# Performance work log

Hardware: AMD Instinct MI355X
Metric: run time of the kernel (lower is better)

Reference implementation:

```python
import jax, jax.numpy as jnp
import numpy as np

N_STEPS = 6
LN_EPS = 1e-5

def _lin(x, w, b):
    # torch Linear: y = x @ W^T + b, w: [out, in]
    return jnp.matmul(x, w.T) + b

def _gelu(x):
    return jax.nn.gelu(x, approximate=False)

def setup_inputs() -> dict:
    key = jax.random.key(0)
    B, T, D, C, V, MS = 8, 1024, 512, 512, 32000, 1024
    ks = jax.random.split(key, 16)
    w = lambda k, shape: (jax.random.normal(k, shape, jnp.float32) * 0.02)
    return {
        "tokens": jax.random.randint(ks[0], (B, T), 0, V),
        "c_states": jax.random.normal(ks[1], (4, C), jnp.float32),
        "embed_w": w(ks[2], (V, D)),
        "pos_w": w(ks[3], (MS, D)),
        "cn_w1": w(ks[4], (2 * D, 4 * D)), "cn_b1": jnp.zeros((2 * D,), jnp.float32),
        "cn_w2": w(ks[5], (D, 2 * D)), "cn_b2": jnp.zeros((D,), jnp.float32),
        "ent_w1": w(ks[6], (64, D)), "ent_b1": jnp.zeros((64,), jnp.float32),
        "ent_w2": w(ks[7], (1, 64)), "ent_b2": jnp.zeros((1,), jnp.float32),
        "ctc_w1": w(ks[8], (2 * D, C)), "ctc_b1": jnp.zeros((2 * D,), jnp.float32),
        "ctc_w2": w(ks[9], (D, 2 * D)), "ctc_b2": jnp.zeros((D,), jnp.float32),
        "base_temp": jnp.asarray(2.0, jnp.float32),
        "ln_g": jnp.ones((D,), jnp.float32), "ln_b": jnp.zeros((D,), jnp.float32),
        "head_w": w(ks[10], (V, D)),
    }

def reference(tokens, c_states, embed_w, pos_w, cn_w1, cn_b1, cn_w2, cn_b2,
              ent_w1, ent_b1, ent_w2, ent_b2, ctc_w1, ctc_b1, ctc_w2, ctc_b2,
              base_temp, ln_g, ln_b, head_w):
    B, T = tokens.shape
    x = embed_w[tokens] + pos_w[:T][None, :, :]          # [B,T,D]
    c_pooled = c_states.mean(axis=0)                      # [C]
    c_constraint = _lin(_gelu(_lin(c_pooled, ctc_w1, ctc_b1)), ctc_w2, ctc_b2)  # [D]
    c_exp = jnp.broadcast_to(c_constraint, (B, T, c_constraint.shape[0]))
    sp_temp = jax.nn.softplus(base_temp)
    for step in range(N_STEPS):
        temp = sp_temp * (1.0 - step / N_STEPS * 0.8)
        left = jnp.roll(x, 1, axis=1)
        right = jnp.roll(x, -1, axis=1)
        ci = jnp.concatenate([x, left, right, c_exp], axis=-1)  # [B,T,4D]
        constraint = _lin(_gelu(_lin(ci, cn_w1, cn_b1)), cn_w2, cn_b2)  # [B,T,D]
        entropy = _lin(_gelu(_lin(x, ent_w1, ent_b1)), ent_w2, ent_b2)[..., 0]  # [B,T]
        cw = jax.nn.softmax(-entropy / temp, axis=-1)            # softmax over T
        x = x + constraint * cw[..., None] * 0.3
    mu = x.mean(axis=-1, keepdims=True)
    var = ((x - mu) ** 2).mean(axis=-1, keepdims=True)
    xn = (x - mu) * jax.lax.rsqrt(var + LN_EPS) * ln_g + ln_b
    return jnp.matmul(xn, head_w.T)                        # [B,T,V]
```

## Files before the change

### kernel.cpp

```cpp
#include <hip/hip_runtime.h>
#include <hip/hip_bf16.h>

typedef __hip_bfloat16 bf16_t;
typedef __bf16 bf16x8_t __attribute__((ext_vector_type(8)));
typedef float f32x4_t __attribute__((ext_vector_type(4)));

#define OFF_X     ((size_t)0)
#define OFF_XB    ((size_t)16777216)
#define OFF_H1    ((size_t)25165824)
#define OFF_XN    ((size_t)41943040)
#define OFF_HEADB ((size_t)50331648)
#define OFF_W1B   ((size_t)83099648)
#define OFF_W2B   ((size_t)86245376)
#define OFF_EW1   ((size_t)87293952)
#define OFF_ENT   ((size_t)87359488)
#define OFF_CW    ((size_t)87392256)
#define OFF_HC    ((size_t)87425024)
#define OFF_CC    ((size_t)87429120)
#define OFF_B1    ((size_t)87431168)

__device__ __forceinline__ float gelu_f(float v) {
    return 0.5f * v * (1.0f + erff(v * 0.7071067811865475f));
}

__device__ __forceinline__ void load_lds16(const bf16_t* g, bf16_t* l) {
    __builtin_amdgcn_global_load_lds(
        (const __attribute__((address_space(1))) void*)g,
        (__attribute__((address_space(3))) void*)l, 16, 0, 0);
}

#define BAR()    __builtin_amdgcn_s_barrier()
#define SCHED0() __builtin_amdgcn_sched_barrier(0)
#define LGKM0()  asm volatile("s_waitcnt lgkmcnt(0)" ::: "memory")
#define WAITV0() asm volatile("s_waitcnt vmcnt(0)" ::: "memory")
#define WAITV2() asm volatile("s_waitcnt vmcnt(2)" ::: "memory")
#define WAITV4() asm volatile("s_waitcnt vmcnt(4)" ::: "memory")

__global__ void prep1_kernel(const float* __restrict__ cs, const float* __restrict__ w1,
                             const float* __restrict__ b1, float* __restrict__ hc) {
    int o = blockIdx.x * 256 + threadIdx.x;
    const float* wr = w1 + (size_t)o * 512;
    float acc = 0.f;
    for (int k = 0; k < 512; k += 4) {
        float4 w4 = *(const float4*)(wr + k);
        float4 a = *(const float4*)(cs + k);
        float4 b = *(const float4*)(cs + 512 + k);
        float4 c = *(const float4*)(cs + 1024 + k);
        float4 d = *(const float4*)(cs + 1536 + k);
        acc += w4.x * (a.x + b.x + c.x + d.x) * 0.25f;
        acc += w4.y * (a.y + b.y + c.y + d.y) * 0.25f;
        acc += w4.z * (a.z + b.z + c.z + d.z) * 0.25f;
        acc += w4.w * (a.w + b.w + c.w + d.w) * 0.25f;
    }
    hc[o] = gelu_f(acc + b1[o]);
}

__global__ void prep2_kernel(const float* __restrict__ hc, const float* __restrict__ w2,
                             const float* __restrict__ b2, float* __restrict__ cc) {
    int o = blockIdx.x * 256 + threadIdx.x;
    const float* wr = w2 + (size_t)o * 1024;
    float acc = 0.f;
    for (int k = 0; k < 1024; ++k) acc += wr[k] * hc[k];
    cc[o] = acc + b2[o];
}

__global__ void prep3_kernel(const float* __restrict__ cc, const float* __restrict__ cn_w1,
                             const float* __restrict__ cn_b1, float* __restrict__ bias1) {
    int o = blockIdx.x * 256 + threadIdx.x;
    const float* wr = cn_w1 + (size_t)o * 2048 + 1536;
    float acc = 0.f;
    for (int k = 0; k < 512; ++k) acc += wr[k] * cc[k];
    bias1[o] = acc + cn_b1[o];
}

__global__ void embed_kernel(const int* __restrict__ tokens, const float* __restrict__ ew,
                             const float* __restrict__ pw, float* __restrict__ x,
                             bf16_t* __restrict__ xb) {
    int idx = blockIdx.x * 256 + threadIdx.x;
    int d4 = idx & 127;
    int bt = idx >> 7;
    int t = bt & 1023;
    int tok = tokens[bt];
    float4 e = ((const float4*)(ew + (size_t)tok * 512))[d4];
    float4 p = ((const float4*)(pw + (size_t)t * 512))[d4];
    float4 o = make_float4(e.x + p.x, e.y + p.y, e.z + p.z, e.w + p.w);
    ((float4*)x)[idx] = o;
    __hip_bfloat162 p0, p1;
    p0.x = __float2bfloat16(o.x); p0.y = __float2bfloat16(o.y);
    p1.x = __float2bfloat16(o.z); p1.y = __float2bfloat16(o.w);
    ((__hip_bfloat162*)xb)[idx * 2]     = p0;
    ((__hip_bfloat162*)xb)[idx * 2 + 1] = p1;
}

__global__ void cvt_kernel(const float* __restrict__ src, bf16_t* __restrict__ dst) {
    int idx = blockIdx.x * 256 + threadIdx.x;
    float4 v = ((const float4*)src)[idx];
    __hip_bfloat162 p0, p1;
    p0.x = __float2bfloat16(v.x); p0.y = __float2bfloat16(v.y);
    p1.x = __float2bfloat16(v.z); p1.y = __float2bfloat16(v.w);
    ((__hip_bfloat162*)dst)[idx * 2]     = p0;
    ((__hip_bfloat162*)dst)[idx * 2 + 1] = p1;
}

__global__ void cvt_w1_kernel(const float* __restrict__ w1, bf16_t* __restrict__ dst) {
    int idx = blockIdx.x * 256 + threadIdx.x;
    int k4 = idx % 384;
    int o = idx / 384;
    float4 v = ((const float4*)(w1 + (size_t)o * 2048))[k4];
    __hip_bfloat162 p0, p1;
    p0.x = __float2bfloat16(v.x); p0.y = __float2bfloat16(v.y);
    p1.x = __float2bfloat16(v.z); p1.y = __float2bfloat16(v.w);
    ((__hip_bfloat162*)dst)[idx * 2]     = p0;
    ((__hip_bfloat162*)dst)[idx * 2 + 1] = p1;
}

__global__ __launch_bounds__(256) void entropy_mfma(
        const bf16_t* __restrict__ xb, const bf16_t* __restrict__ w1b,
        const float* __restrict__ b1, const float* __restrict__ w2,
        const float* __restrict__ b2, float* __restrict__ ent) {
    int wave = threadIdx.x >> 6, lane = threadIdx.x & 63;
    int lr = lane & 15, kq = lane >> 4;
    int tok0 = (blockIdx.x * 4 + wave) * 16;
    f32x4_t acc[4] = {};
    const bf16_t* xr = xb + (size_t)(tok0 + lr) * 512 + kq * 8;
    const bf16_t* wr = w1b + (size_t)lr * 512 + kq * 8;
    #pragma unroll 4
    for (int k0 = 0; k0 < 512; k0 += 32) {
        bf16x8_t a = *(const bf16x8_t*)(xr + k0);
        #pragma unroll
        for (int j = 0; j < 4; ++j) {
            bf16x8_t bb = *(const bf16x8_t*)(wr + (size_t)j * 16 * 512 + k0);
            acc[j] = __builtin_amdgcn_mfma_f32_16x16x32_bf16(a, bb, acc[j], 0, 0, 0);
        }
    }
    float p[4];
    #pragma unroll
    for (int r = 0; r < 4; ++r) {
        float s = 0.f;
        #pragma unroll
        for (int j = 0; j < 4; ++j) {
            int n = j * 16 + lr;
            s += gelu_f(acc[j][r] + b1[n]) * w2[n];
        }
        #pragma unroll
        for (int o = 1; o < 16; o <<= 1) s += __shfl_xor(s, o);
        p[r] = s;
    }
    if (lr == 0) {
        float bb = b2[0];
        #pragma unroll
        for (int r = 0; r < 4; ++r) ent[tok0 + kq * 4 + r] = p[r] + bb;
    }
}

__global__ void softmax_kernel(const float* __restrict__ ent, const float* __restrict__ btp,
                               float stepf, float* __restrict__ cw) {
    __shared__ float red[16];
    __shared__ float bc[2];
    int b = blockIdx.x, t = threadIdx.x;
    float bt = btp[0];
    float sp = (bt > 20.0f) ? bt : log1pf(expf(bt));
    float inv = -1.0f / (sp * stepf);
    float v = ent[b * 1024 + t] * inv;
    float m = v;
    #pragma unroll
    for (int o = 32; o; o >>= 1) m = fmaxf(m, __shfl_xor(m, o));
    if ((t & 63) == 0) red[t >> 6] = m;
    __syncthreads();
    if (t < 64) {
        float mm = (t < 16) ? red[t] : -3.4e38f;
        #pragma unroll
        for (int o = 32; o; o >>= 1) mm = fmaxf(mm, __shfl_xor(mm, o));
        if (t == 0) bc[0] = mm;
    }
    __syncthreads();
    float e = expf(v - bc[0]);
    float s = e;
    #pragma unroll
    for (int o = 32; o; o >>= 1) s += __shfl_xor(s, o);
    if ((t & 63) == 0) red[t >> 6] = s;
    __syncthreads();
    if (t < 64) {
        float ss = (t < 16) ? red[t] : 0.f;
        #pragma unroll
        for (int o = 32; o; o >>= 1) ss += __shfl_xor(ss, o);
        if (t == 0) bc[1] = ss;
    }
    __syncthreads();
    cw[b * 1024 + t] = e / bc[1];
}

__global__ void ln_kernel(const float* __restrict__ x, const float* __restrict__ g,
                          const float* __restrict__ b, bf16_t* __restrict__ xn) {
    int token = blockIdx.x * 4 + (threadIdx.x >> 6);
    int l = threadIdx.x & 63;
    const float* xr = x + (size_t)token * 512;
    float4 v0 = ((const float4*)xr)[l * 2];
    float4 v1 = ((const float4*)xr)[l * 2 + 1];
    float s = v0.x + v0.y + v0.z + v0.w + v1.x + v1.y + v1.z + v1.w;
    float ss = v0.x * v0.x + v0.y * v0.y + v0.z * v0.z + v0.w * v0.w
             + v1.x * v1.x + v1.y * v1.y + v1.z * v1.z + v1.w * v1.w;
    #pragma unroll
    for (int o = 32; o; o >>= 1) { s += __shfl_xor(s, o); ss += __shfl_xor(ss, o); }
    float mu = s * (1.0f / 512.0f);
    float var = ss * (1.0f / 512.0f) - mu * mu;
    float rs = rsqrtf(var + 1e-5f);
    float4 g0 = ((const float4*)g)[l * 2], g1 = ((const float4*)g)[l * 2 + 1];
    float4 b0 = ((const float4*)b)[l * 2], b1 = ((const float4*)b)[l * 2 + 1];
    bf16_t* op = xn + (size_t)token * 512 + l * 8;
    op[0] = __float2bfloat16((v0.x - mu) * rs * g0.x + b0.x);
    op[1] = __float2bfloat16((v0.y - mu) * rs * g0.y + b0.y);
    op[2] = __float2bfloat16((v0.z - mu) * rs * g0.z + b0.z);
    op[3] = __float2bfloat16((v0.w - mu) * rs * g0.w + b0.w);
    op[4] = __float2bfloat16((v1.x - mu) * rs * g1.x + b1.x);
    op[5] = __float2bfloat16((v1.y - mu) * rs * g1.y + b1.y);
    op[6] = __float2bfloat16((v1.z - mu) * rs * g1.z + b1.z);
    op[7] = __float2bfloat16((v1.w - mu) * rs * g1.w + b1.w);
}

template <int MODE, int ROLL, int BN>
__global__ __launch_bounds__(512, 2) void gemm8p(
    const bf16_t* __restrict__ A, int lda,
    const bf16_t* __restrict__ B, int ldb, int K, int NMT,
    const float* __restrict__ bias,
    bf16_t* __restrict__ out_bf, int ldc,
    const float* __restrict__ cw, float* __restrict__ x,
    float* __restrict__ out_f)
{
    constexpr int JJ = BN / 64;
    __shared__ __align__(16) bf16_t As[2][256 * 64];
    __shared__ __align__(16) bf16_t Bs[2][BN * 64];

    const int NT = K >> 6;
    const int nwg = gridDim.x;
    const int id0 = blockIdx.x;
    const int id = (id0 & 7) * (nwg >> 3) + (id0 >> 3);
    const int m0 = (id % NMT) * 256;
    const int n0 = (id / NMT) * BN;

    const int tid = threadIdx.x;
    const int wave = tid >> 6, lane = tid & 63;
    const int wm = (wave >> 2) * 128;
    const int wn = (wave & 3) * (BN / 4);
    const int lr = lane & 15, kq = lane >> 4;

    const int swz0 = (kq)     ^ (lr & 7);
    const int swz1 = (4 + kq) ^ (lr & 7);
    const int eoff0 = lr * 64 + swz0 * 8;
    const int eoff1 = lr * 64 + swz1 * 8;

    const int u0row = tid >> 3;
    const int u1row = 64 + (tid >> 3);
    const int usl   = tid & 7;
    const int c0 = ((usl ^ (u0row & 7)) * 8);
    const int c1 = ((usl ^ (u1row & 7)) * 8);

    f32x4_t acc[8][JJ] = {};
    bf16x8_t bfr[JJ][2];

    auto stageA = [&](int ktile, int c, int half) {
        const int kbase = ktile << 6;
        const int r0 = m0 + half * 128 + u0row;
        const int r1 = m0 + half * 128 + u1row;
        const bf16_t *g0, *g1;
        if (ROLL) {
            const int seg = kbase >> 9;
            const int kk2 = kbase & 511;
            const int sh = (seg == 0) ? 0 : ((seg == 1) ? 1023 : 1);
            const int s0 = (r0 & ~1023) | (((r0 & 1023) + sh) & 1023);
            const int s1 = (r1 & ~1023) | (((r1 & 1023) + sh) & 1023);
            g0 = A + (size_t)s0 * 512 + kk2 + c0;
            g1 = A + (size_t)s1 * 512 + kk2 + c1;
        } else {
            g0 = A + (size_t)r0 * lda + kbase + c0;
            g1 = A + (size_t)r1 * lda + kbase + c1;
        }
        bf16_t* l = &As[c][half * 128 * 64];
        load_lds16(g0, l + tid * 8);
        load_lds16(g1, l + (tid + 512) * 8);
    };
    auto stageB = [&](int ktile, int c, int half) {
        const int kbase = ktile << 6;
        const int r0 = n0 + half * 128 + u0row;
        const int r1 = n0 + half * 128 + u1row;
        const bf16_t* g0 = B + (size_t)r0 * ldb + kbase + c0;
        const bf16_t* g1 = B + (size_t)r1 * ldb + kbase + c1;
        bf16_t* l = &Bs[c][half * 128 * 64];
        load_lds16(g0, l + tid * 8);
        load_lds16(g1, l + (tid + 512) * 8);
    };

    stageA(0, 0, 0); stageA(0, 0, 1);
    stageB(0, 0, 0); if (BN == 256) stageB(0, 0, 1);
    stageB(1, 1, 0); if (BN == 256) stageB(1, 1, 1);
    if (BN == 256) { WAITV4(); } else { WAITV2(); }
    BAR();

    int cur = 0;
    for (int t = 0; t < NT; ++t) {
        #pragma unroll
        for (int p = 0; p < 4; ++p) {
            bf16x8_t af0k0, af0k1, af1k0, af1k1;
            {
                const int r0 = (wm + 32 * p + lr) * 64;
                const int r1 = (wm + 32 * p + 16 + lr) * 64;
                af0k0 = *(const bf16x8_t*)&As[cur][r0 - lr * 64 + eoff0];
                af0k1 = *(const bf16x8_t*)&As[cur][r0 - lr * 64 + eoff1];
                af1k0 = *(const bf16x8_t*)&As[cur][r1 - lr * 64 + eoff0];
                af1k1 = *(const bf16x8_t*)&As[cur][r1 - lr * 64 + eoff1];
            }
            if (p == 0) {
                #pragma unroll
                for (int j = 0; j < JJ; ++j) {
                    const int rb = (wn + 16 * j) * 64;
                    bfr[j][0] = *(const bf16x8_t*)&Bs[cur][rb + eoff0];
                    bfr[j][1] = *(const bf16x8_t*)&Bs[cur][rb + eoff1];
                }
            }
            if (p == 0 && t + 1 < NT) stageA(t + 1, cur ^ 1, 0);
            if (p == 1 && t + 1 < NT) stageA(t + 1, cur ^ 1, 1);
            if (p == 2 && t + 2 < NT) stageB(t + 2, cur, 0);
            if (p == 3 && BN == 256 && t + 2 < NT) stageB(t + 2, cur, 1);

            BAR();
            LGKM0();
            SCHED0();
            __builtin_amdgcn_s_setprio(1);
            #pragma unroll
            for (int j = 0; j < JJ; ++j) {
                acc[2*p][j]   = __builtin_amdgcn_mfma_f32_16x16x32_bf16(af0k0, bfr[j][0], acc[2*p][j],   0, 0, 0);
                acc[2*p+1][j] = __builtin_amdgcn_mfma_f32_16x16x32_bf16(af1k0, bfr[j][0], acc[2*p+1][j], 0, 0, 0);
            }
            #pragma unroll
            for (int j = 0; j < JJ; ++j) {
                acc[2*p][j]   = __builtin_amdgcn_mfma_f32_16x16x32_bf16(af0k1, bfr[j][1], acc[2*p][j],   0, 0, 0);
                acc[2*p+1][j] = __builtin_amdgcn_mfma_f32_16x16x32_bf16(af1k1, bfr[j][1], acc[2*p+1][j], 0, 0, 0);
            }
            __builtin_amdgcn_s_setprio(0);
            SCHED0();
            if (p == 3) {
                if (t + 2 < NT) { if (BN == 256) { WAITV4(); } else { WAITV2(); } }
                else           { WAITV0(); }
            }
            BAR();
        }
        cur ^= 1;
    }

    #pragma unroll
    for (int i = 0; i < 8; ++i) {
        const int rbase = m0 + wm + i * 16 + kq * 4;
        #pragma unroll
        for (int j = 0; j < JJ; ++j) {
            const int gcol = n0 + wn + j * 16 + lr;
            #pragma unroll
            for (int r = 0; r < 4; ++r) {
                const size_t grow = (size_t)(rbase + r);
                float v = acc[i][j][r];
                if (MODE == 0) {
                    v = gelu_f(v + bias[gcol]);
                    out_bf[grow * ldc + gcol] = __float2bfloat16(v);
                } else if (MODE == 1) {
                    v += bias[gcol];
                    float nv = x[grow * ldc + gcol] + v * cw[grow] * 0.3f;
                    x[grow * ldc + gcol] = nv;
                    out_bf[grow * ldc + gcol] = __float2bfloat16(nv);
                } else {
                    out_f[grow * ldc + gcol] = v;
                }
            }
        }
    }
}

extern "C" void kernel_launch(void* const* d_in, const int* in_sizes, int n_in,
                              void* d_out, int out_size, void* d_ws, size_t ws_size,
                              hipStream_t stream) {
    const int*   tokens   = (const int*)d_in[0];
    const float* c_states = (const float*)d_in[1];
    const float* embed_w  = (const float*)d_in[2];
    const float* pos_w    = (const float*)d_in[3];
    const float* cn_w1    = (const float*)d_in[4];
    const float* cn_b1    = (const float*)d_in[5];
    const float* cn_w2    = (const float*)d_in[6];
    const float* cn_b2    = (const float*)d_in[7];
    const float* ent_w1   = (const float*)d_in[8];
    const float* ent_b1   = (const float*)d_in[9];
    const float* ent_w2   = (const float*)d_in[10];
    const float* ent_b2   = (const float*)d_in[11];
    const float* ctc_w1   = (const float*)d_in[12];
    const float* ctc_b1   = (const float*)d_in[13];
    const float* ctc_w2   = (const float*)d_in[14];
    const float* ctc_b2   = (const float*)d_in[15];
    const float* base_temp= (const float*)d_in[16];
    const float* ln_g     = (const float*)d_in[17];
    const float* ln_b     = (const float*)d_in[18];
    const float* head_w   = (const float*)d_in[19];
    float* out = (float*)d_out;

    char* ws = (char*)d_ws;
    float*  x     = (float*)(ws + OFF_X);
    bf16_t* xb    = (bf16_t*)(ws + OFF_XB);
    bf16_t* h1    = (bf16_t*)(ws + OFF_H1);
    bf16_t* xn    = (bf16_t*)(ws + OFF_XN);
    bf16_t* headb = (bf16_t*)(ws + OFF_HEADB);
    bf16_t* w1b   = (bf16_t*)(ws + OFF_W1B);
    bf16_t* w2b   = (bf16_t*)(ws + OFF_W2B);
    bf16_t* ew1b  = (bf16_t*)(ws + OFF_EW1);
    float*  ent   = (float*)(ws + OFF_ENT);
    float*  cw    = (float*)(ws + OFF_CW);
    float*  hc    = (float*)(ws + OFF_HC);
    float*  cc    = (float*)(ws + OFF_CC);
    float*  bias1 = (float*)(ws + OFF_B1);

    cvt_w1_kernel<<<1536, 256, 0, stream>>>(cn_w1, w1b);
    cvt_kernel<<<512, 256, 0, stream>>>(cn_w2, w2b);
    cvt_kernel<<<32, 256, 0, stream>>>(ent_w1, ew1b);
    prep1_kernel<<<4, 256, 0, stream>>>(c_states, ctc_w1, ctc_b1, hc);
    prep2_kernel<<<2, 256, 0, stream>>>(hc, ctc_w2, ctc_b2, cc);
    prep3_kernel<<<4, 256, 0, stream>>>(cc, cn_w1, cn_b1, bias1);
    embed_kernel<<<4096, 256, 0, stream>>>(tokens, embed_w, pos_w, x, xb);

    for (int step = 0; step < 6; ++step) {
        float stepf = 1.0f - ((float)step / 6.0f) * 0.8f;
        entropy_mfma<<<128, 256, 0, stream>>>(xb, ew1b, ent_b1, ent_w2, ent_b2, ent);
        softmax_kernel<<<8, 1024, 0, stream>>>(ent, base_temp, stepf, cw);
        gemm8p<0, 1, 128><<<256, 512, 0, stream>>>(xb, 512, w1b, 1536, 1536, 32,
                                                   bias1, h1, 1024, nullptr, nullptr, nullptr);
        gemm8p<1, 0, 128><<<128, 512, 0, stream>>>(h1, 1024, w2b, 1024, 1024, 32,
                                                   cn_b2, xb, 512, cw, x, nullptr);
    }

    cvt_kernel<<<16000, 256, 0, stream>>>(head_w, headb);
    ln_kernel<<<2048, 256, 0, stream>>>(x, ln_g, ln_b, xn);
    gemm8p<2, 0, 256><<<4000, 512, 0, stream>>>(xn, 512, headb, 512, 512, 32,
                                                nullptr, nullptr, 32000, nullptr, nullptr, out);
}
```

Baseline: 1.205 ms.

## Fuse entropy into first GEMM, softmax into second, merge prep and convert kernels

The entropy MLP now runs as extra workgroups appended to the first constraint GEMM launch. Each block of the second GEMM recomputes the per-batch softmax over T from the entropy values and keeps its slice of the weights in shared memory. This removes two launches per step and the cw buffer round trip. The three small prep matvecs become one single-block kernel that holds intermediates in LDS, and all weight conversions merge into one launch. The cost is redundant softmax work in every GEMM block, plus a serial single-block prep kernel.

```diff
diff --git a/kernel.cpp b/kernel.cpp
--- a/kernel.cpp
+++ b/kernel.cpp
@@ -14,10 +14,7 @@
 #define OFF_W2B   ((size_t)86245376)
 #define OFF_EW1   ((size_t)87293952)
 #define OFF_ENT   ((size_t)87359488)
-#define OFF_CW    ((size_t)87392256)
-#define OFF_HC    ((size_t)87425024)
-#define OFF_CC    ((size_t)87429120)
-#define OFF_B1    ((size_t)87431168)
+#define OFF_B1    ((size_t)87425024)
 
 __device__ __forceinline__ float gelu_f(float v) {
     return 0.5f * v * (1.0f + erff(v * 0.7071067811865475f));
@@ -36,41 +33,45 @@
 #define WAITV2() asm volatile("s_waitcnt vmcnt(2)" ::: "memory")
 #define WAITV4() asm volatile("s_waitcnt vmcnt(4)" ::: "memory")
 
-__global__ void prep1_kernel(const float* __restrict__ cs, const float* __restrict__ w1,
-                             const float* __restrict__ b1, float* __restrict__ hc) {
-    int o = blockIdx.x * 256 + threadIdx.x;
-    const float* wr = w1 + (size_t)o * 512;
-    float acc = 0.f;
-    for (int k = 0; k < 512; k += 4) {
-        float4 w4 = *(const float4*)(wr + k);
-        float4 a = *(const float4*)(cs + k);
-        float4 b = *(const float4*)(cs + 512 + k);
-        float4 c = *(const float4*)(cs + 1024 + k);
-        float4 d = *(const float4*)(cs + 1536 + k);
-        acc += w4.x * (a.x + b.x + c.x + d.x) * 0.25f;
-        acc += w4.y * (a.y + b.y + c.y + d.y) * 0.25f;
-        acc += w4.z * (a.z + b.z + c.z + d.z) * 0.25f;
-        acc += w4.w * (a.w + b.w + c.w + d.w) * 0.25f;
-    }
-    hc[o] = gelu_f(acc + b1[o]);
-}
-
-__global__ void prep2_kernel(const float* __restrict__ hc, const float* __restrict__ w2,
-                             const float* __restrict__ b2, float* __restrict__ cc) {
-    int o = blockIdx.x * 256 + threadIdx.x;
-    const float* wr = w2 + (size_t)o * 1024;
-    float acc = 0.f;
-    for (int k = 0; k < 1024; ++k) acc += wr[k] * hc[k];
-    cc[o] = acc + b2[o];
-}
-
-__global__ void prep3_kernel(const float* __restrict__ cc, const float* __restrict__ cn_w1,
-                             const float* __restrict__ cn_b1, float* __restrict__ bias1) {
-    int o = blockIdx.x * 256 + threadIdx.x;
-    const float* wr = cn_w1 + (size_t)o * 2048 + 1536;
-    float acc = 0.f;
-    for (int k = 0; k < 512; ++k) acc += wr[k] * cc[k];
-    bias1[o] = acc + cn_b1[o];
+__global__ __launch_bounds__(1024) void prep_all(
+        const float* __restrict__ cs,
+        const float* __restrict__ ctc_w1, const float* __restrict__ ctc_b1,
+        const float* __restrict__ ctc_w2, const float* __restrict__ ctc_b2,
+        const float* __restrict__ cn_w1, const float* __restrict__ cn_b1,
+        float* __restrict__ bias1) {
+    __shared__ float hc_s[1024];
+    __shared__ float cc_s[512];
+    int o = threadIdx.x;
+    {
+        const float* wr = ctc_w1 + (size_t)o * 512;
+        float acc = 0.f;
+        for (int k = 0; k < 512; k += 4) {
+            float4 w4 = *(const float4*)(wr + k);
+            float4 a = *(const float4*)(cs + k);
+            float4 b = *(const float4*)(cs + 512 + k);
+            float4 c = *(const float4*)(cs + 1024 + k);
+            float4 d = *(const float4*)(cs + 1536 + k);
+            acc += w4.x * (a.x + b.x + c.x + d.x) * 0.25f;
+            acc += w4.y * (a.y + b.y + c.y + d.y) * 0.25f;
+            acc += w4.z * (a.z + b.z + c.z + d.z) * 0.25f;
+            acc += w4.w * (a.w + b.w + c.w + d.w) * 0.25f;
+        }
+        hc_s[o] = gelu_f(acc + ctc_b1[o]);
+    }
+    __syncthreads();
+    if (o < 512) {
+        const float* wr = ctc_w2 + (size_t)o * 1024;
+        float acc = 0.f;
+        for (int k = 0; k < 1024; ++k) acc += wr[k] * hc_s[k];
+        cc_s[o] = acc + ctc_b2[o];
+    }
+    __syncthreads();
+    {
+        const float* wr = cn_w1 + (size_t)o * 2048 + 1536;
+        float acc = 0.f;
+        for (int k = 0; k < 512; ++k) acc += wr[k] * cc_s[k];
+        bias1[o] = acc + cn_b1[o];
+    }
 }
 
 __global__ void embed_kernel(const int* __restrict__ tokens, const float* __restrict__ ew,
@@ -92,102 +93,37 @@
     ((__hip_bfloat162*)xb)[idx * 2 + 1] = p1;
 }
 
-__global__ void cvt_kernel(const float* __restrict__ src, bf16_t* __restrict__ dst) {
-    int idx = blockIdx.x * 256 + threadIdx.x;
-    float4 v = ((const float4*)src)[idx];
+__device__ __forceinline__ void cvt_store(const float4 v, __hip_bfloat162* dst) {
     __hip_bfloat162 p0, p1;
     p0.x = __float2bfloat16(v.x); p0.y = __float2bfloat16(v.y);
     p1.x = __float2bfloat16(v.z); p1.y = __float2bfloat16(v.w);
-    ((__hip_bfloat162*)dst)[idx * 2]     = p0;
-    ((__hip_bfloat162*)dst)[idx * 2 + 1] = p1;
-}
-
-__global__ void cvt_w1_kernel(const float* __restrict__ w1, bf16_t* __restrict__ dst) {
-    int idx = blockIdx.x * 256 + threadIdx.x;
-    int k4 = idx % 384;
-    int o = idx / 384;
-    float4 v = ((const float4*)(w1 + (size_t)o * 2048))[k4];
-    __hip_bfloat162 p0, p1;
-    p0.x = __float2bfloat16(v.x); p0.y = __float2bfloat16(v.y);
-    p1.x = __float2bfloat16(v.z); p1.y = __float2bfloat16(v.w);
-    ((__hip_bfloat162*)dst)[idx * 2]     = p0;
-    ((__hip_bfloat162*)dst)[idx * 2 + 1] = p1;
-}
-
-__global__ __launch_bounds__(256) void entropy_mfma(
-        const bf16_t* __restrict__ xb, const bf16_t* __restrict__ w1b,
-        const float* __restrict__ b1, const float* __restrict__ w2,
-        const float* __restrict__ b2, float* __restrict__ ent) {
-    int wave = threadIdx.x >> 6, lane = threadIdx.x & 63;
-    int lr = lane & 15, kq = lane >> 4;
-    int tok0 = (blockIdx.x * 4 + wave) * 16;
-    f32x4_t acc[4] = {};
-    const bf16_t* xr = xb + (size_t)(tok0 + lr) * 512 + kq * 8;
-    const bf16_t* wr = w1b + (size_t)lr * 512 + kq * 8;
-    #pragma unroll 4
-    for (int k0 = 0; k0 < 512; k0 += 32) {
-        bf16x8_t a = *(const bf16x8_t*)(xr + k0);
-        #pragma unroll
-        for (int j = 0; j < 4; ++j) {
-            bf16x8_t bb = *(const bf16x8_t*)(wr + (size_t)j * 16 * 512 + k0);
-            acc[j] = __builtin_amdgcn_mfma_f32_16x16x32_bf16(a, bb, acc[j], 0, 0, 0);
-        }
-    }
-    float p[4];
-    #pragma unroll
-    for (int r = 0; r < 4; ++r) {
-        float s = 0.f;
-        #pragma unroll
-        for (int j = 0; j < 4; ++j) {
-            int n = j * 16 + lr;
-            s += gelu_f(acc[j][r] + b1[n]) * w2[n];
-        }
-        #pragma unroll
-        for (int o = 1; o < 16; o <<= 1) s += __shfl_xor(s, o);
-        p[r] = s;
-    }
-    if (lr == 0) {
-        float bb = b2[0];
-        #pragma unroll
-        for (int r = 0; r < 4; ++r) ent[tok0 + kq * 4 + r] = p[r] + bb;
-    }
-}
-
-__global__ void softmax_kernel(const float* __restrict__ ent, const float* __restrict__ btp,
-                               float stepf, float* __restrict__ cw) {
-    __shared__ float red[16];
-    __shared__ float bc[2];
-    int b = blockIdx.x, t = threadIdx.x;
-    float bt = btp[0];
-    float sp = (bt > 20.0f) ? bt : log1pf(expf(bt));
-    float inv = -1.0f / (sp * stepf);
-    float v = ent[b * 1024 + t] * inv;
-    float m = v;
-    #pragma unroll
-    for (int o = 32; o; o >>= 1) m = fmaxf(m, __shfl_xor(m, o));
-    if ((t & 63) == 0) red[t >> 6] = m;
-    __syncthreads();
-    if (t < 64) {
-        float mm = (t < 16) ? red[t] : -3.4e38f;
-        #pragma unroll
-        for (int o = 32; o; o >>= 1) mm = fmaxf(mm, __shfl_xor(mm, o));
-        if (t == 0) bc[0] = mm;
-    }
-    __syncthreads();
-    float e = expf(v - bc[0]);
-    float s = e;
-    #pragma unroll
-    for (int o = 32; o; o >>= 1) s += __shfl_xor(s, o);
-    if ((t & 63) == 0) red[t >> 6] = s;
-    __syncthreads();
-    if (t < 64) {
-        float ss = (t < 16) ? red[t] : 0.f;
-        #pragma unroll
-        for (int o = 32; o; o >>= 1) ss += __shfl_xor(ss, o);
-        if (t == 0) bc[1] = ss;
-    }
-    __syncthreads();
-    cw[b * 1024 + t] = e / bc[1];
+    dst[0] = p0; dst[1] = p1;
+}
+
+__global__ void cvt_all_kernel(const float* __restrict__ cn_w1, const float* __restrict__ cn_w2,
+                               const float* __restrict__ ent_w1, const float* __restrict__ head_w,
+                               bf16_t* __restrict__ w1b, bf16_t* __restrict__ w2b,
+                               bf16_t* __restrict__ ew1b, bf16_t* __restrict__ headb) {
+    int bid = blockIdx.x;
+    if (bid < 1536) {
+        int idx = bid * 256 + threadIdx.x;
+        int k4 = idx % 384;
+        int o = idx / 384;
+        float4 v = ((const float4*)(cn_w1 + (size_t)o * 2048))[k4];
+        cvt_store(v, (__hip_bfloat162*)w1b + idx * 2);
+    } else if (bid < 2048) {
+        int idx = (bid - 1536) * 256 + threadIdx.x;
+        float4 v = ((const float4*)cn_w2)[idx];
+        cvt_store(v, (__hip_bfloat162*)w2b + idx * 2);
+    } else if (bid < 2080) {
+        int idx = (bid - 2048) * 256 + threadIdx.x;
+        float4 v = ((const float4*)ent_w1)[idx];
+        cvt_store(v, (__hip_bfloat162*)ew1b + idx * 2);
+    } else {
+        int idx = (bid - 2080) * 256 + threadIdx.x;
+        float4 v = ((const float4*)head_w)[idx];
+        cvt_store(v, (__hip_bfloat162*)headb + idx * 2);
+    }
 }
 
 __global__ void ln_kernel(const float* __restrict__ x, const float* __restrict__ g,
@@ -218,31 +154,112 @@
     op[7] = __float2bfloat16((v1.w - mu) * rs * g1.w + b1.w);
 }
 
-template <int MODE, int ROLL, int BN>
+template <int MODE, int ROLL, int BN, int FUSE_ENT>
 __global__ __launch_bounds__(512, 2) void gemm8p(
     const bf16_t* __restrict__ A, int lda,
-    const bf16_t* __restrict__ B, int ldb, int K, int NMT,
+    const bf16_t* __restrict__ B, int ldb, int K, int NMT, int ngemm,
     const float* __restrict__ bias,
     bf16_t* __restrict__ out_bf, int ldc,
-    const float* __restrict__ cw, float* __restrict__ x,
-    float* __restrict__ out_f)
+    float* __restrict__ x, float* __restrict__ out_f,
+    const bf16_t* __restrict__ ew1b, const float* __restrict__ eb1,
+    const float* __restrict__ ew2, const float* __restrict__ eb2,
+    float* __restrict__ entp,
+    const float* __restrict__ btp, float stepf)
 {
     constexpr int JJ = BN / 64;
     __shared__ __align__(16) bf16_t As[2][256 * 64];
     __shared__ __align__(16) bf16_t Bs[2][BN * 64];
+    __shared__ float cwb[256];
+    __shared__ float sred[8];
+    __shared__ float sbc[2];
+
+    const int tid = threadIdx.x;
+    const int wave = tid >> 6, lane = tid & 63;
+    const int lr = lane & 15, kq = lane >> 4;
+
+    if (FUSE_ENT && (int)blockIdx.x >= ngemm) {
+        int tok0 = (((int)blockIdx.x - ngemm) * 8 + wave) * 16;
+        f32x4_t acc[4] = {};
+        const bf16_t* xr = A + (size_t)(tok0 + lr) * 512 + kq * 8;
+        const bf16_t* wr = ew1b + (size_t)lr * 512 + kq * 8;
+        #pragma unroll 4
+        for (int k0 = 0; k0 < 512; k0 += 32) {
+            bf16x8_t a = *(const bf16x8_t*)(xr + k0);
+            #pragma unroll
+            for (int j = 0; j < 4; ++j) {
+                bf16x8_t bb = *(const bf16x8_t*)(wr + (size_t)j * 16 * 512 + k0);
+                acc[j] = __builtin_amdgcn_mfma_f32_16x16x32_bf16(a, bb, acc[j], 0, 0, 0);
+            }
+        }
+        float p[4];
+        #pragma unroll
+        for (int r = 0; r < 4; ++r) {
+            float s = 0.f;
+            #pragma unroll
+            for (int j = 0; j < 4; ++j) {
+                int n = j * 16 + lr;
+                s += gelu_f(acc[j][r] + eb1[n]) * ew2[n];
+            }
+            #pragma unroll
+            for (int o = 1; o < 16; o <<= 1) s += __shfl_xor(s, o);
+            p[r] = s;
+        }
+        if (lr == 0) {
+            float bb = eb2[0];
+            #pragma unroll
+            for (int r = 0; r < 4; ++r) entp[tok0 + kq * 4 + r] = p[r] + bb;
+        }
+        return;
+    }
 
     const int NT = K >> 6;
-    const int nwg = gridDim.x;
     const int id0 = blockIdx.x;
-    const int id = (id0 & 7) * (nwg >> 3) + (id0 >> 3);
+    const int id = (id0 & 7) * (ngemm >> 3) + (id0 >> 3);
     const int m0 = (id % NMT) * 256;
     const int n0 = (id / NMT) * BN;
 
-    const int tid = threadIdx.x;
-    const int wave = tid >> 6, lane = tid & 63;
+    if (MODE == 1) {
+        const float* eb = entp + (size_t)(m0 >> 10) * 1024;
+        float bt = btp[0];
+        float sp = (bt > 20.0f) ? bt : log1pf(expf(bt));
+        float inv = -1.0f / (sp * stepf);
+        float v0 = eb[tid] * inv;
+        float v1 = eb[tid + 512] * inv;
+        float mx = fmaxf(v0, v1);
+        #pragma unroll
+        for (int o = 32; o; o >>= 1) mx = fmaxf(mx, __shfl_xor(mx, o));
+        if (lane == 0) sred[wave] = mx;
+        __syncthreads();
+        if (tid < 64) {
+            float mm = (tid < 8) ? sred[tid] : -3.4e38f;
+            #pragma unroll
+            for (int o = 4; o; o >>= 1) mm = fmaxf(mm, __shfl_xor(mm, o));
+            if (tid == 0) sbc[0] = mm;
+        }
+        __syncthreads();
+        float M = sbc[0];
+        float e0 = expf(v0 - M), e1 = expf(v1 - M);
+        float s = e0 + e1;
+        #pragma unroll
+        for (int o = 32; o; o >>= 1) s += __shfl_xor(s, o);
+        if (lane == 0) sred[wave] = s;
+        __syncthreads();
+        if (tid < 64) {
+            float ssum = (tid < 8) ? sred[tid] : 0.f;
+            #pragma unroll
+            for (int o = 4; o; o >>= 1) ssum += __shfl_xor(ssum, o);
+            if (tid == 0) sbc[1] = ssum;
+        }
+        __syncthreads();
+        float S = sbc[1];
+        int t0 = m0 & 1023;
+        if ((unsigned)(tid - t0) < 256u)       cwb[tid - t0] = e0 / S;
+        if ((unsigned)(tid + 512 - t0) < 256u) cwb[tid + 512 - t0] = e1 / S;
+        __syncthreads();
+    }
+
     const int wm = (wave >> 2) * 128;
     const int wn = (wave & 3) * (BN / 4);
-    const int lr = lane & 15, kq = lane >> 4;
 
     const int swz0 = (kq)     ^ (lr & 7);
     const int swz1 = (4 + kq) ^ (lr & 7);
@@ -362,7 +379,7 @@
                     out_bf[grow * ldc + gcol] = __float2bfloat16(v);
                 } else if (MODE == 1) {
                     v += bias[gcol];
-                    float nv = x[grow * ldc + gcol] + v * cw[grow] * 0.3f;
+                    float nv = x[grow * ldc + gcol] + v * cwb[(int)grow - m0] * 0.3f;
                     x[grow * ldc + gcol] = nv;
                     out_bf[grow * ldc + gcol] = __float2bfloat16(nv);
                 } else {
@@ -408,31 +425,29 @@
     bf16_t* w2b   = (bf16_t*)(ws + OFF_W2B);
     bf16_t* ew1b  = (bf16_t*)(ws + OFF_EW1);
     float*  ent   = (float*)(ws + OFF_ENT);
-    float*  cw    = (float*)(ws + OFF_CW);
-    float*  hc    = (float*)(ws + OFF_HC);
-    float*  cc    = (float*)(ws + OFF_CC);
     float*  bias1 = (float*)(ws + OFF_B1);
 
-    cvt_w1_kernel<<<1536, 256, 0, stream>>>(cn_w1, w1b);
-    cvt_kernel<<<512, 256, 0, stream>>>(cn_w2, w2b);
-    cvt_kernel<<<32, 256, 0, stream>>>(ent_w1, ew1b);
-    prep1_kernel<<<4, 256, 0, stream>>>(c_states, ctc_w1, ctc_b1, hc);
-    prep2_kernel<<<2, 256, 0, stream>>>(hc, ctc_w2, ctc_b2, cc);
-    prep3_kernel<<<4, 256, 0, stream>>>(cc, cn_w1, cn_b1, bias1);
+    cvt_all_kernel<<<18080, 256, 0, stream>>>(cn_w1, cn_w2, ent_w1, head_w,
+                                              w1b, w2b, ew1b, headb);
+    prep_all<<<1, 1024, 0, stream>>>(c_states, ctc_w1, ctc_b1, ctc_w2, ctc_b2,
+                                     cn_w1, cn_b1, bias1);
     embed_kernel<<<4096, 256, 0, stream>>>(tokens, embed_w, pos_w, x, xb);
 
     for (int step = 0; step < 6; ++step) {
         float stepf = 1.0f - ((float)step / 6.0f) * 0.8f;
-        entropy_mfma<<<128, 256, 0, stream>>>(xb, ew1b, ent_b1, ent_w2, ent_b2, ent);
-        softmax_kernel<<<8, 1024, 0, stream>>>(ent, base_temp, stepf, cw);
-        gemm8p<0, 1, 128><<<256, 512, 0, stream>>>(xb, 512, w1b, 1536, 1536, 32,
-                                                   bias1, h1, 1024, nullptr, nullptr, nullptr);
-        gemm8p<1, 0, 128><<<128, 512, 0, stream>>>(h1, 1024, w2b, 1024, 1024, 32,
-                                                   cn_b2, xb, 512, cw, x, nullptr);
-    }
-
-    cvt_kernel<<<16000, 256, 0, stream>>>(head_w, headb);
+        gemm8p<0, 1, 128, 1><<<320, 512, 0, stream>>>(
+            xb, 512, w1b, 1536, 1536, 32, 256,
+            bias1, h1, 1024, nullptr, nullptr,
+            ew1b, ent_b1, ent_w2, ent_b2, ent, nullptr, 0.f);
+        gemm8p<1, 0, 128, 0><<<128, 512, 0, stream>>>(
+            h1, 1024, w2b, 1024, 1024, 32, 128,
+            cn_b2, xb, 512, x, nullptr,
+            nullptr, nullptr, nullptr, nullptr, ent, base_temp, stepf);
+    }
+
     ln_kernel<<<2048, 256, 0, stream>>>(x, ln_g, ln_b, xn);
-    gemm8p<2, 0, 256><<<4000, 512, 0, stream>>>(xn, 512, headb, 512, 512, 32,
-                                                nullptr, nullptr, 32000, nullptr, nullptr, out);
-}
+    gemm8p<2, 0, 256, 0><<<4000, 512, 0, stream>>>(
+        xn, 512, headb, 512, 512, 32, 4000,
+        nullptr, nullptr, 32000, nullptr, out,
+        nullptr, nullptr, nullptr, nullptr, nullptr, nullptr, 0.f);
+}
```

Result: slower. 1.425 ms (+18.3%).

## Merge weight conversions and prep kernels; restructure BN=128 GEMM main loop

Applied to the files above, without the earlier changes.

Fuses all fp32-to-bf16 weight conversions, including head_w, into one launch, and merges the three tiny constraint-bias kernels into a single 1024-thread block that keeps its intermediates in shared memory. This cuts launch count and global round trips for small vectors. The BN=128 GEMM path now runs two phases of four A-row groups per k-tile instead of four phases of two, which halves the barriers per tile. The larger A fragment working set raises register pressure, and the single-block prep kernel uses only one CU.

```diff
diff --git a/kernel.cpp b/kernel.cpp
--- a/kernel.cpp
+++ b/kernel.cpp
@@ -15,9 +15,7 @@
 #define OFF_EW1   ((size_t)87293952)
 #define OFF_ENT   ((size_t)87359488)
 #define OFF_CW    ((size_t)87392256)
-#define OFF_HC    ((size_t)87425024)
-#define OFF_CC    ((size_t)87429120)
-#define OFF_B1    ((size_t)87431168)
+#define OFF_B1    ((size_t)87425024)
 
 __device__ __forceinline__ float gelu_f(float v) {
     return 0.5f * v * (1.0f + erff(v * 0.7071067811865475f));
@@ -36,41 +34,45 @@
 #define WAITV2() asm volatile("s_waitcnt vmcnt(2)" ::: "memory")
 #define WAITV4() asm volatile("s_waitcnt vmcnt(4)" ::: "memory")
 
-__global__ void prep1_kernel(const float* __restrict__ cs, const float* __restrict__ w1,
-                             const float* __restrict__ b1, float* __restrict__ hc) {
-    int o = blockIdx.x * 256 + threadIdx.x;
-    const float* wr = w1 + (size_t)o * 512;
-    float acc = 0.f;
-    for (int k = 0; k < 512; k += 4) {
-        float4 w4 = *(const float4*)(wr + k);
-        float4 a = *(const float4*)(cs + k);
-        float4 b = *(const float4*)(cs + 512 + k);
-        float4 c = *(const float4*)(cs + 1024 + k);
-        float4 d = *(const float4*)(cs + 1536 + k);
-        acc += w4.x * (a.x + b.x + c.x + d.x) * 0.25f;
-        acc += w4.y * (a.y + b.y + c.y + d.y) * 0.25f;
-        acc += w4.z * (a.z + b.z + c.z + d.z) * 0.25f;
-        acc += w4.w * (a.w + b.w + c.w + d.w) * 0.25f;
-    }
-    hc[o] = gelu_f(acc + b1[o]);
-}
-
-__global__ void prep2_kernel(const float* __restrict__ hc, const float* __restrict__ w2,
-                             const float* __restrict__ b2, float* __restrict__ cc) {
-    int o = blockIdx.x * 256 + threadIdx.x;
-    const float* wr = w2 + (size_t)o * 1024;
-    float acc = 0.f;
-    for (int k = 0; k < 1024; ++k) acc += wr[k] * hc[k];
-    cc[o] = acc + b2[o];
-}
-
-__global__ void prep3_kernel(const float* __restrict__ cc, const float* __restrict__ cn_w1,
-                             const float* __restrict__ cn_b1, float* __restrict__ bias1) {
-    int o = blockIdx.x * 256 + threadIdx.x;
-    const float* wr = cn_w1 + (size_t)o * 2048 + 1536;
-    float acc = 0.f;
-    for (int k = 0; k < 512; ++k) acc += wr[k] * cc[k];
-    bias1[o] = acc + cn_b1[o];
+__global__ __launch_bounds__(1024) void prep_all(
+        const float* __restrict__ cs,
+        const float* __restrict__ ctc_w1, const float* __restrict__ ctc_b1,
+        const float* __restrict__ ctc_w2, const float* __restrict__ ctc_b2,
+        const float* __restrict__ cn_w1, const float* __restrict__ cn_b1,
+        float* __restrict__ bias1) {
+    __shared__ float hc_s[1024];
+    __shared__ float cc_s[512];
+    int o = threadIdx.x;
+    {
+        const float* wr = ctc_w1 + (size_t)o * 512;
+        float acc = 0.f;
+        for (int k = 0; k < 512; k += 4) {
+            float4 w4 = *(const float4*)(wr + k);
+            float4 a = *(const float4*)(cs + k);
+            float4 b = *(const float4*)(cs + 512 + k);
+            float4 c = *(const float4*)(cs + 1024 + k);
+            float4 d = *(const float4*)(cs + 1536 + k);
+            acc += w4.x * (a.x + b.x + c.x + d.x) * 0.25f;
+            acc += w4.y * (a.y + b.y + c.y + d.y) * 0.25f;
+            acc += w4.z * (a.z + b.z + c.z + d.z) * 0.25f;
+            acc += w4.w * (a.w + b.w + c.w + d.w) * 0.25f;
+        }
+        hc_s[o] = gelu_f(acc + ctc_b1[o]);
+    }
+    __syncthreads();
+    if (o < 512) {
+        const float* wr = ctc_w2 + (size_t)o * 1024;
+        float acc = 0.f;
+        for (int k = 0; k < 1024; ++k) acc += wr[k] * hc_s[k];
+        cc_s[o] = acc + ctc_b2[o];
+    }
+    __syncthreads();
+    {
+        const float* wr = cn_w1 + (size_t)o * 2048 + 1536;
+        float acc = 0.f;
+        for (int k = 0; k < 512; ++k) acc += wr[k] * cc_s[k];
+        bias1[o] = acc + cn_b1[o];
+    }
 }
 
 __global__ void embed_kernel(const int* __restrict__ tokens, const float* __restrict__ ew,
@@ -92,26 +94,37 @@
     ((__hip_bfloat162*)xb)[idx * 2 + 1] = p1;
 }
 
-__global__ void cvt_kernel(const float* __restrict__ src, bf16_t* __restrict__ dst) {
-    int idx = blockIdx.x * 256 + threadIdx.x;
-    float4 v = ((const float4*)src)[idx];
+__device__ __forceinline__ void cvt_store(const float4 v, __hip_bfloat162* dst) {
     __hip_bfloat162 p0, p1;
     p0.x = __float2bfloat16(v.x); p0.y = __float2bfloat16(v.y);
     p1.x = __float2bfloat16(v.z); p1.y = __float2bfloat16(v.w);
-    ((__hip_bfloat162*)dst)[idx * 2]     = p0;
-    ((__hip_bfloat162*)dst)[idx * 2 + 1] = p1;
-}
-
-__global__ void cvt_w1_kernel(const float* __restrict__ w1, bf16_t* __restrict__ dst) {
-    int idx = blockIdx.x * 256 + threadIdx.x;
-    int k4 = idx % 384;
-    int o = idx / 384;
-    float4 v = ((const float4*)(w1 + (size_t)o * 2048))[k4];
-    __hip_bfloat162 p0, p1;
-    p0.x = __float2bfloat16(v.x); p0.y = __float2bfloat16(v.y);
-    p1.x = __float2bfloat16(v.z); p1.y = __float2bfloat16(v.w);
-    ((__hip_bfloat162*)dst)[idx * 2]     = p0;
-    ((__hip_bfloat162*)dst)[idx * 2 + 1] = p1;
+    dst[0] = p0; dst[1] = p1;
+}
+
+__global__ void cvt_all_kernel(const float* __restrict__ cn_w1, const float* __restrict__ cn_w2,
+                               const float* __restrict__ ent_w1, const float* __restrict__ head_w,
+                               bf16_t* __restrict__ w1b, bf16_t* __restrict__ w2b,
+                               bf16_t* __restrict__ ew1b, bf16_t* __restrict__ headb) {
+    int bid = blockIdx.x;
+    if (bid < 1536) {
+        int idx = bid * 256 + threadIdx.x;
+        int k4 = idx % 384;
+        int o = idx / 384;
+        float4 v = ((const float4*)(cn_w1 + (size_t)o * 2048))[k4];
+        cvt_store(v, (__hip_bfloat162*)w1b + idx * 2);
+    } else if (bid < 2048) {
+        int idx = (bid - 1536) * 256 + threadIdx.x;
+        float4 v = ((const float4*)cn_w2)[idx];
+        cvt_store(v, (__hip_bfloat162*)w2b + idx * 2);
+    } else if (bid < 2080) {
+        int idx = (bid - 2048) * 256 + threadIdx.x;
+        float4 v = ((const float4*)ent_w1)[idx];
+        cvt_store(v, (__hip_bfloat162*)ew1b + idx * 2);
+    } else {
+        int idx = (bid - 2080) * 256 + threadIdx.x;
+        float4 v = ((const float4*)head_w)[idx];
+        cvt_store(v, (__hip_bfloat162*)headb + idx * 2);
+    }
 }
 
 __global__ __launch_bounds__(256) void entropy_mfma(
@@ -297,54 +310,98 @@
     BAR();
 
     int cur = 0;
-    for (int t = 0; t < NT; ++t) {
-        #pragma unroll
-        for (int p = 0; p < 4; ++p) {
-            bf16x8_t af0k0, af0k1, af1k0, af1k1;
-            {
-                const int r0 = (wm + 32 * p + lr) * 64;
-                const int r1 = (wm + 32 * p + 16 + lr) * 64;
-                af0k0 = *(const bf16x8_t*)&As[cur][r0 - lr * 64 + eoff0];
-                af0k1 = *(const bf16x8_t*)&As[cur][r0 - lr * 64 + eoff1];
-                af1k0 = *(const bf16x8_t*)&As[cur][r1 - lr * 64 + eoff0];
-                af1k1 = *(const bf16x8_t*)&As[cur][r1 - lr * 64 + eoff1];
-            }
-            if (p == 0) {
+    if (BN == 256) {
+        for (int t = 0; t < NT; ++t) {
+            #pragma unroll
+            for (int p = 0; p < 4; ++p) {
+                bf16x8_t af0k0, af0k1, af1k0, af1k1;
+                af0k0 = *(const bf16x8_t*)&As[cur][(wm + 32 * p) * 64 + eoff0];
+                af0k1 = *(const bf16x8_t*)&As[cur][(wm + 32 * p) * 64 + eoff1];
+                af1k0 = *(const bf16x8_t*)&As[cur][(wm + 32 * p + 16) * 64 + eoff0];
+                af1k1 = *(const bf16x8_t*)&As[cur][(wm + 32 * p + 16) * 64 + eoff1];
+                if (p == 0) {
+                    #pragma unroll
+                    for (int j = 0; j < JJ; ++j) {
+                        bfr[j][0] = *(const bf16x8_t*)&Bs[cur][(wn + 16 * j) * 64 + eoff0];
+                        bfr[j][1] = *(const bf16x8_t*)&Bs[cur][(wn + 16 * j) * 64 + eoff1];
+                    }
+                }
+                if (p == 0 && t + 1 < NT) stageA(t + 1, cur ^ 1, 0);
+                if (p == 1 && t + 1 < NT) stageA(t + 1, cur ^ 1, 1);
+                if (p == 2 && t + 2 < NT) stageB(t + 2, cur, 0);
+                if (p == 3 && t + 2 < NT) stageB(t + 2, cur, 1);
+
+                BAR();
+                LGKM0();
+                SCHED0();
+                __builtin_amdgcn_s_setprio(1);
                 #pragma unroll
                 for (int j = 0; j < JJ; ++j) {
-                    const int rb = (wn + 16 * j) * 64;
-                    bfr[j][0] = *(const bf16x8_t*)&Bs[cur][rb + eoff0];
-                    bfr[j][1] = *(const bf16x8_t*)&Bs[cur][rb + eoff1];
-                }
+                    acc[2*p][j]   = __builtin_amdgcn_mfma_f32_16x16x32_bf16(af0k0, bfr[j][0], acc[2*p][j],   0, 0, 0);
+                    acc[2*p+1][j] = __builtin_amdgcn_mfma_f32_16x16x32_bf16(af1k0, bfr[j][0], acc[2*p+1][j], 0, 0, 0);
+                }
+                #pragma unroll
+                for (int j = 0; j < JJ; ++j) {
+                    acc[2*p][j]   = __builtin_amdgcn_mfma_f32_16x16x32_bf16(af0k1, bfr[j][1], acc[2*p][j],   0, 0, 0);
+                    acc[2*p+1][j] = __builtin_amdgcn_mfma_f32_16x16x32_bf16(af1k1, bfr[j][1], acc[2*p+1][j], 0, 0, 0);
+                }
+                __builtin_amdgcn_s_setprio(0);
+                SCHED0();
+                if (p == 3) {
+                    if (t + 2 < NT) { WAITV4(); }
+                    else            { WAITV0(); }
+                }
+                BAR();
             }
-            if (p == 0 && t + 1 < NT) stageA(t + 1, cur ^ 1, 0);
-            if (p == 1 && t + 1 < NT) stageA(t + 1, cur ^ 1, 1);
-            if (p == 2 && t + 2 < NT) stageB(t + 2, cur, 0);
-            if (p == 3 && BN == 256 && t + 2 < NT) stageB(t + 2, cur, 1);
-
-            BAR();
-            LGKM0();
-            SCHED0();
-            __builtin_amdgcn_s_setprio(1);
+            cur ^= 1;
+        }
+    } else {
+        for (int t = 0; t < NT; ++t) {
             #pragma unroll
-            for (int j = 0; j < JJ; ++j) {
-                acc[2*p][j]   = __builtin_amdgcn_mfma_f32_16x16x32_bf16(af0k0, bfr[j][0], acc[2*p][j],   0, 0, 0);
-                acc[2*p+1][j] = __builtin_amdgcn_mfma_f32_16x16x32_bf16(af1k0, bfr[j][0], acc[2*p+1][j], 0, 0, 0);
+            for (int p = 0; p < 2; ++p) {
+                bf16x8_t af[4][2];
+                #pragma unroll
+                for (int q = 0; q < 4; ++q) {
+                    af[q][0] = *(const bf16x8_t*)&As[cur][(wm + 64 * p + 16 * q) * 64 + eoff0];
+                    af[q][1] = *(const bf16x8_t*)&As[cur][(wm + 64 * p + 16 * q) * 64 + eoff1];
+                }
+                if (p == 0) {
+                    #pragma unroll
+                    for (int j = 0; j < JJ; ++j) {
+                        bfr[j][0] = *(const bf16x8_t*)&Bs[cur][(wn + 16 * j) * 64 + eoff0];
+                        bfr[j][1] = *(const bf16x8_t*)&Bs[cur][(wn + 16 * j) * 64 + eoff1];
+                    }
+                }
+                if (p == 0 && t + 1 < NT) stageA(t + 1, cur ^ 1, 0);
+                if (p == 1) {
+                    if (t + 1 < NT) stageA(t + 1, cur ^ 1, 1);
+                    if (t + 2 < NT) stageB(t + 2, cur, 0);
+                }
+
+                BAR();
+                LGKM0();
+                SCHED0();
+                __builtin_amdgcn_s_setprio(1);
+                #pragma unroll
+                for (int q = 0; q < 4; ++q)
+                    #pragma unroll
+                    for (int j = 0; j < JJ; ++j)
+                        acc[4*p+q][j] = __builtin_amdgcn_mfma_f32_16x16x32_bf16(af[q][0], bfr[j][0], acc[4*p+q][j], 0, 0, 0);
+                #pragma unroll
+                for (int q = 0; q < 4; ++q)
+                    #pragma unroll
+                    for (int j = 0; j < JJ; ++j)
+                        acc[4*p+q][j] = __builtin_amdgcn_mfma_f32_16x16x32_bf16(af[q][1], bfr[j][1], acc[4*p+q][j], 0, 0, 0);
+                __builtin_amdgcn_s_setprio(0);
+                SCHED0();
+                if (p == 1) {
+                    if (t + 2 < NT)      { WAITV2(); }
+                    else if (t + 1 < NT) { WAITV0(); }
+                }
+                BAR();
             }
-            #pragma unroll
-            for (int j = 0; j < JJ; ++j) {
-                acc[2*p][j]   = __builtin_amdgcn_mfma_f32_16x16x32_bf16(af0k1, bfr[j][1], acc[2*p][j],   0, 0, 0);
-                acc[2*p+1][j] = __builtin_amdgcn_mfma_f32_16x16x32_bf16(af1k1, bfr[j][1], acc[2*p+1][j], 0, 0, 0);
-            }
-            __builtin_amdgcn_s_setprio(0);
-            SCHED0();
-            if (p == 3) {
-                if (t + 2 < NT) { if (BN == 256) { WAITV4(); } else { WAITV2(); } }
-                else           { WAITV0(); }
-            }
-            BAR();
-        }
-        cur ^= 1;
+            cur ^= 1;
+        }
     }
 
     #pragma unroll
@@ -409,16 +466,12 @@
     bf16_t* ew1b  = (bf16_t*)(ws + OFF_EW1);
     float*  ent   = (float*)(ws + OFF_ENT);
     float*  cw    = (float*)(ws + OFF_CW);
-    float*  hc    = (float*)(ws + OFF_HC);
-    float*  cc    = (float*)(ws + OFF_CC);
     float*  bias1 = (float*)(ws + OFF_B1);
 
-    cvt_w1_kernel<<<1536, 256, 0, stream>>>(cn_w1, w1b);
-    cvt_kernel<<<512, 256, 0, stream>>>(cn_w2, w2b);
-    cvt_kernel<<<32, 256, 0, stream>>>(ent_w1, ew1b);
-    prep1_kernel<<<4, 256, 0, stream>>>(c_states, ctc_w1, ctc_b1, hc);
-    prep2_kernel<<<2, 256, 0, stream>>>(hc, ctc_w2, ctc_b2, cc);
-    prep3_kernel<<<4, 256, 0, stream>>>(cc, cn_w1, cn_b1, bias1);
+    cvt_all_kernel<<<18080, 256, 0, stream>>>(cn_w1, cn_w2, ent_w1, head_w,
+                                              w1b, w2b, ew1b, headb);
+    prep_all<<<1, 1024, 0, stream>>>(c_states, ctc_w1, ctc_b1, ctc_w2, ctc_b2,
+                                     cn_w1, cn_b1, bias1);
     embed_kernel<<<4096, 256, 0, stream>>>(tokens, embed_w, pos_w, x, xb);
 
     for (int step = 0; step < 6; ++step) {
@@ -431,7 +484,6 @@
                                                    cn_b2, xb, 512, cw, x, nullptr);
     }
 
-    cvt_kernel<<<16000, 256, 0, stream>>>(head_w, headb);
     ln_kernel<<<2048, 256, 0, stream>>>(x, ln_g, ln_b, xn);
     gemm8p<2, 0, 256><<<4000, 512, 0, stream>>>(xn, 512, headb, 512, 512, 32,
                                                 nullptr, nullptr, 32000, nullptr, nullptr, out);
```

Result: slower. 1.369 ms (+13.6%).
